# Performance work log

Measured on AMD Instinct MI355X. Metric: run time of the kernel, lower is better.

Reference implementation:

```python
import jax, jax.numpy as jnp
import numpy as np

N_NODES = 500000
EMB = 32
K = 10          # sampled neighbors per node (num_sample in source)
BATCH = 100000


def setup_inputs() -> dict:
    key = jax.random.key(0)
    k1, k2, k3, k4, k5 = jax.random.split(key, 5)
    # xavier-ish scale for weights [emb, 2*emb]
    w_scale = jnp.sqrt(2.0 / (EMB + 2 * EMB)).astype(jnp.float32)
    emb = jax.random.normal(k1, (N_NODES, EMB), dtype=jnp.float32)
    W1 = jax.random.normal(k2, (EMB, 2 * EMB), dtype=jnp.float32) * w_scale
    W2 = jax.random.normal(k3, (EMB, 2 * EMB), dtype=jnp.float32) * w_scale
    node_batch = jax.random.randint(k4, (BATCH,), 0, N_NODES)
    neigh = jax.random.randint(k5, (N_NODES, K), 0, N_NODES)
    return {"emb": emb, "W1": W1, "W2": W2,
            "node_batch": node_batch, "neigh": neigh}


def _sage_layer(self_feat, agg_feat, W):
    # SageLayer.forward: relu(W.mm(cat([self, agg], 1).t()).t()) == relu(cat @ W.T)
    combined = jnp.concatenate([self_feat, agg_feat], axis=1)  # [n, 2E]
    return jax.nn.relu(combined @ W.T)                          # [n, E]


def reference(emb, W1, W2, node_batch, neigh):
    # Layer 1: MEAN aggregation of K sampled neighbors for every node
    # (mask.mm(embed_matrix) with row-normalized 0/1 mask == gather + mean)
    agg1 = jnp.take(emb, neigh, axis=0).mean(axis=1)   # [N, E]
    h1 = _sage_layer(emb, agg1, W1)                    # [N, E]
    # Layer 2: aggregate over neighbors of the batch nodes using layer-1 embeds
    nb_neigh = jnp.take(neigh, node_batch, axis=0)     # [B, K]
    agg2 = jnp.take(h1, nb_neigh, axis=0).mean(axis=1) # [B, E]
    out = _sage_layer(jnp.take(h1, node_batch, axis=0), agg2, W2)  # [B, E]
    return out
```

## Files before the change

kernel.cpp:

```cpp
#include <hip/hip_runtime.h>

#define EMBD 32
#define KN 10

__device__ __forceinline__ float bf2f(unsigned short u) {
    union { unsigned int u; float f; } c; c.u = ((unsigned int)u) << 16; return c.f;
}
__device__ __forceinline__ unsigned short f2bf(float f) {
    union { float f; unsigned int u; } c; c.f = f;
    unsigned int u = c.u + 0x7FFFu + ((c.u >> 16) & 1u);
    return (unsigned short)(u >> 16);
}

__global__ __launch_bounds__(256)
void cvt_bf16_kernel(const float4* __restrict__ in, ushort4* __restrict__ out, int n4)
{
    int i = blockIdx.x * 256 + threadIdx.x;
    if (i < n4) {
        float4 v = in[i];
        ushort4 o;
        o.x = f2bf(v.x); o.y = f2bf(v.y); o.z = f2bf(v.z); o.w = f2bf(v.w);
        out[i] = o;
    }
}

template<bool REMAP, bool OUT_BF16>
__global__ __launch_bounds__(256, 4)
void sage_layer(const unsigned short* __restrict__ feat,
                const float* __restrict__ W,
                const int*   __restrict__ neigh,
                const int*   __restrict__ remap,
                void*        __restrict__ out,
                int n_rows)
{
    __shared__ float sh[64][65];
    const int tid  = threadIdx.x;
    const int row0 = blockIdx.x << 6;

    {
        const int hw = tid >> 5;
        const int j  = tid & 31;
        #pragma unroll 2
        for (int i = 0; i < 8; ++i) {
            const int rl = hw * 8 + i;
            int r = row0 + rl;
            if (r >= n_rows) r = n_rows - 1;
            const int node = REMAP ? remap[r] : r;
            const float self = bf2f(feat[node * EMBD + j]);
            const int* nb = neigh + node * KN;
            float agg = 0.f;
            #pragma unroll
            for (int k = 0; k < KN; ++k)
                agg += bf2f(feat[nb[k] * EMBD + j]);
            sh[j][rl]      = self;
            sh[32 + j][rl] = agg * 0.1f;
        }
    }
    __syncthreads();

    const int row = tid & 63;
    const int wid = __builtin_amdgcn_readfirstlane(tid >> 6);
    const float* Wb = W + wid * 8 * 64;

    float acc[8] = {0.f,0.f,0.f,0.f,0.f,0.f,0.f,0.f};
    #pragma unroll 8
    for (int jj = 0; jj < 64; ++jj) {
        const float c = sh[jj][row];
        #pragma unroll
        for (int q = 0; q < 8; ++q)
            acc[q] = fmaf(c, Wb[q * 64 + jj], acc[q]);
    }

    const int r = row0 + row;
    if (r < n_rows) {
        if (OUT_BF16) {
            unsigned int pk[4];
            #pragma unroll
            for (int q = 0; q < 4; ++q) {
                float a0 = fmaxf(acc[2*q],     0.f);
                float a1 = fmaxf(acc[2*q + 1], 0.f);
                pk[q] = (unsigned int)f2bf(a0) | ((unsigned int)f2bf(a1) << 16);
            }
            uint4* dst = (uint4*)((unsigned short*)out + (size_t)r * EMBD + wid * 8);
            *dst = make_uint4(pk[0], pk[1], pk[2], pk[3]);
        } else {
            float* dst = (float*)out + (size_t)r * EMBD + wid * 8;
            ((float4*)dst)[0] = make_float4(fmaxf(acc[0],0.f), fmaxf(acc[1],0.f),
                                            fmaxf(acc[2],0.f), fmaxf(acc[3],0.f));
            ((float4*)dst)[1] = make_float4(fmaxf(acc[4],0.f), fmaxf(acc[5],0.f),
                                            fmaxf(acc[6],0.f), fmaxf(acc[7],0.f));
        }
    }
}

extern "C" void kernel_launch(void* const* d_in, const int* in_sizes, int n_in,
                              void* d_out, int out_size, void* d_ws, size_t ws_size,
                              hipStream_t stream)
{
    const float* emb        = (const float*)d_in[0];
    const float* W1         = (const float*)d_in[1];
    const float* W2         = (const float*)d_in[2];
    const int*   node_batch = (const int*)  d_in[3];
    const int*   neigh      = (const int*)  d_in[4];

    const int N = in_sizes[0] / EMBD;
    const int B = in_sizes[3];

    unsigned short* emb_bf = (unsigned short*)d_ws;
    unsigned short* h1_bf  = emb_bf + (size_t)N * EMBD;

    const int n4 = (N * EMBD) / 4;
    cvt_bf16_kernel<<<(n4 + 255) / 256, 256, 0, stream>>>(
        (const float4*)emb, (ushort4*)emb_bf, n4);

    sage_layer<false, true><<<(N + 63) / 64, 256, 0, stream>>>(
        emb_bf, W1, neigh, nullptr, (void*)h1_bf, N);

    sage_layer<true, false><<<(B + 63) / 64, 256, 0, stream>>>(
        h1_bf, W2, neigh, node_batch, d_out, B);
}
```

Baseline: 236.5 us.

## Restructure SAGE gathers with staged indices and 8-byte nontemporal row loads

```diff
diff --git a/kernel.cpp b/kernel.cpp
--- a/kernel.cpp
+++ b/kernel.cpp
@@ -3,93 +3,188 @@
 #define EMBD 32
 #define KN 10
 
-__device__ __forceinline__ float bf2f(unsigned short u) {
-    union { unsigned int u; float f; } c; c.u = ((unsigned int)u) << 16; return c.f;
-}
-__device__ __forceinline__ unsigned short f2bf(float f) {
-    union { float f; unsigned int u; } c; c.f = f;
-    unsigned int u = c.u + 0x7FFFu + ((c.u >> 16) & 1u);
-    return (unsigned short)(u >> 16);
+__device__ __forceinline__ float bf_lo(unsigned int u){ union{unsigned int v; float f;}c; c.v = u<<16; return c.f; }
+__device__ __forceinline__ float bf_hi(unsigned int u){ union{unsigned int v; float f;}c; c.v = u & 0xFFFF0000u; return c.f; }
+__device__ __forceinline__ unsigned short f2bf(float f){
+    union{float f; unsigned int u;}c; c.f=f;
+    unsigned int r = c.u + 0x7FFFu + ((c.u>>16)&1u);
+    return (unsigned short)(r>>16);
+}
+__device__ __forceinline__ void ld_nt4bf(const unsigned short* p,
+                                         float& f0, float& f1, float& f2, float& f3){
+    unsigned long long v = __builtin_nontemporal_load((const unsigned long long*)p);
+    unsigned int lo = (unsigned int)v, hi = (unsigned int)(v >> 32);
+    f0 = bf_lo(lo); f1 = bf_hi(lo); f2 = bf_lo(hi); f3 = bf_hi(hi);
 }
 
 __global__ __launch_bounds__(256)
-void cvt_bf16_kernel(const float4* __restrict__ in, ushort4* __restrict__ out, int n4)
+void cvt_bf16(const float4* __restrict__ in, ushort4* __restrict__ out, int n4){
+    int i = blockIdx.x*256 + threadIdx.x;
+    if (i < n4){
+        float4 v = in[i];
+        ushort4 o; o.x=f2bf(v.x); o.y=f2bf(v.y); o.z=f2bf(v.z); o.w=f2bf(v.w);
+        out[i]=o;
+    }
+}
+
+__global__ __launch_bounds__(256, 6)
+void sage_l1(const float* __restrict__ emb,
+             const unsigned short* __restrict__ embb,
+             const float* __restrict__ W,
+             const int* __restrict__ neigh,
+             unsigned short* __restrict__ h1,
+             int n_rows)
 {
-    int i = blockIdx.x * 256 + threadIdx.x;
-    if (i < n4) {
-        float4 v = in[i];
-        ushort4 o;
-        o.x = f2bf(v.x); o.y = f2bf(v.y); o.z = f2bf(v.z); o.w = f2bf(v.w);
-        out[i] = o;
-    }
-}
-
-template<bool REMAP, bool OUT_BF16>
-__global__ __launch_bounds__(256, 4)
-void sage_layer(const unsigned short* __restrict__ feat,
-                const float* __restrict__ W,
-                const int*   __restrict__ neigh,
-                const int*   __restrict__ remap,
-                void*        __restrict__ out,
-                int n_rows)
-{
-    __shared__ float sh[64][65];
+    __shared__ __align__(16) int sidx[64*KN];
+    __shared__ float sagg[64][33];
     const int tid  = threadIdx.x;
     const int row0 = blockIdx.x << 6;
 
-    {
-        const int hw = tid >> 5;
-        const int j  = tid & 31;
-        #pragma unroll 2
-        for (int i = 0; i < 8; ++i) {
-            const int rl = hw * 8 + i;
-            int r = row0 + rl;
-            if (r >= n_rows) r = n_rows - 1;
-            const int node = REMAP ? remap[r] : r;
-            const float self = bf2f(feat[node * EMBD + j]);
-            const int* nb = neigh + node * KN;
-            float agg = 0.f;
-            #pragma unroll
-            for (int k = 0; k < KN; ++k)
-                agg += bf2f(feat[nb[k] * EMBD + j]);
-            sh[j][rl]      = self;
-            sh[32 + j][rl] = agg * 0.1f;
-        }
-    }
-    __syncthreads();
-
-    const int row = tid & 63;
-    const int wid = __builtin_amdgcn_readfirstlane(tid >> 6);
-    const float* Wb = W + wid * 8 * 64;
-
-    float acc[8] = {0.f,0.f,0.f,0.f,0.f,0.f,0.f,0.f};
+    if (row0 + 64 <= n_rows) {
+        if (tid < 160)
+            ((int4*)sidx)[tid] = ((const int4*)(neigh + (size_t)row0*KN))[tid];
+    } else {
+        for (int t = tid; t < 64*KN; t += 256) {
+            int lr = t / KN;
+            sidx[t] = (row0 + lr < n_rows) ? neigh[(size_t)row0*KN + t] : 0;
+        }
+    }
+    __syncthreads();
+
+    const int lane = tid & 63;
+    const int wv   = tid >> 6;
+    const int slot = lane & 7;
+    const int rsub = lane >> 3;
+
+    #pragma unroll
+    for (int gi = 0; gi < 2; ++gi) {
+        const int row = (2*wv + gi)*8 + rsub;
+        float a0=0.f,a1=0.f,a2=0.f,a3=0.f;
+        #pragma unroll
+        for (int k = 0; k < KN; ++k) {
+            const int idx = sidx[row*KN + k];
+            float f0,f1,f2,f3;
+            ld_nt4bf(embb + (size_t)idx*EMBD + slot*4, f0,f1,f2,f3);
+            a0 += f0; a1 += f1; a2 += f2; a3 += f3;
+        }
+        sagg[row][slot*4+0] = a0*0.1f;
+        sagg[row][slot*4+1] = a1*0.1f;
+        sagg[row][slot*4+2] = a2*0.1f;
+        sagg[row][slot*4+3] = a3*0.1f;
+    }
+    __syncthreads();
+
+    const int row = lane;
+    const int r   = row0 + row;
+    const int rc  = (r < n_rows) ? r : (n_rows - 1);
+    const float* selfrow = emb + (size_t)rc * EMBD;
+    const float* Wb = W + wv*8*64;
+
+    float acc[8] = {0,0,0,0,0,0,0,0};
+    #pragma unroll
+    for (int c4 = 0; c4 < 8; ++c4) {
+        const float4 s = ((const float4*)selfrow)[c4];
+        #pragma unroll
+        for (int q = 0; q < 8; ++q) {
+            acc[q] = fmaf(s.x, Wb[q*64 + c4*4 + 0], acc[q]);
+            acc[q] = fmaf(s.y, Wb[q*64 + c4*4 + 1], acc[q]);
+            acc[q] = fmaf(s.z, Wb[q*64 + c4*4 + 2], acc[q]);
+            acc[q] = fmaf(s.w, Wb[q*64 + c4*4 + 3], acc[q]);
+        }
+    }
     #pragma unroll 8
-    for (int jj = 0; jj < 64; ++jj) {
-        const float c = sh[jj][row];
+    for (int j = 0; j < 32; ++j) {
+        const float c = sagg[row][j];
         #pragma unroll
         for (int q = 0; q < 8; ++q)
-            acc[q] = fmaf(c, Wb[q * 64 + jj], acc[q]);
-    }
-
-    const int r = row0 + row;
+            acc[q] = fmaf(c, Wb[q*64 + 32 + j], acc[q]);
+    }
     if (r < n_rows) {
-        if (OUT_BF16) {
-            unsigned int pk[4];
-            #pragma unroll
-            for (int q = 0; q < 4; ++q) {
-                float a0 = fmaxf(acc[2*q],     0.f);
-                float a1 = fmaxf(acc[2*q + 1], 0.f);
-                pk[q] = (unsigned int)f2bf(a0) | ((unsigned int)f2bf(a1) << 16);
-            }
-            uint4* dst = (uint4*)((unsigned short*)out + (size_t)r * EMBD + wid * 8);
-            *dst = make_uint4(pk[0], pk[1], pk[2], pk[3]);
-        } else {
-            float* dst = (float*)out + (size_t)r * EMBD + wid * 8;
-            ((float4*)dst)[0] = make_float4(fmaxf(acc[0],0.f), fmaxf(acc[1],0.f),
-                                            fmaxf(acc[2],0.f), fmaxf(acc[3],0.f));
-            ((float4*)dst)[1] = make_float4(fmaxf(acc[4],0.f), fmaxf(acc[5],0.f),
-                                            fmaxf(acc[6],0.f), fmaxf(acc[7],0.f));
-        }
+        unsigned int pk[4];
+        #pragma unroll
+        for (int q = 0; q < 4; ++q) {
+            float x0 = fmaxf(acc[2*q],0.f), x1 = fmaxf(acc[2*q+1],0.f);
+            pk[q] = (unsigned int)f2bf(x0) | ((unsigned int)f2bf(x1)<<16);
+        }
+        *(uint4*)(h1 + (size_t)r*EMBD + wv*8) = make_uint4(pk[0],pk[1],pk[2],pk[3]);
+    }
+}
+
+__global__ __launch_bounds__(256, 6)
+void sage_l2(const unsigned short* __restrict__ h1,
+             const float* __restrict__ W,
+             const int* __restrict__ neigh,
+             const int* __restrict__ batch,
+             float* __restrict__ out,
+             int n_rows)
+{
+    __shared__ int snode[64];
+    __shared__ __align__(16) int sidx[64*KN];
+    __shared__ float sh[64][67];
+    const int tid  = threadIdx.x;
+    const int row0 = blockIdx.x << 6;
+
+    if (tid < 64) {
+        int r = row0 + tid;
+        snode[tid] = (r < n_rows) ? batch[r] : 0;
+    }
+    __syncthreads();
+    for (int t = tid; t < 64*KN; t += 256) {
+        int lr = t / KN;
+        int k  = t - lr*KN;
+        sidx[t] = neigh[(size_t)snode[lr]*KN + k];
+    }
+    __syncthreads();
+
+    const int lane = tid & 63;
+    const int wv   = tid >> 6;
+    const int slot = lane & 7;
+    const int rsub = lane >> 3;
+
+    #pragma unroll
+    for (int gi = 0; gi < 2; ++gi) {
+        const int row = (2*wv + gi)*8 + rsub;
+        {
+            const int node = snode[row];
+            float f0,f1,f2,f3;
+            ld_nt4bf(h1 + (size_t)node*EMBD + slot*4, f0,f1,f2,f3);
+            sh[row][slot*4+0] = f0;
+            sh[row][slot*4+1] = f1;
+            sh[row][slot*4+2] = f2;
+            sh[row][slot*4+3] = f3;
+        }
+        float a0=0.f,a1=0.f,a2=0.f,a3=0.f;
+        #pragma unroll
+        for (int k = 0; k < KN; ++k) {
+            const int idx = sidx[row*KN + k];
+            float f0,f1,f2,f3;
+            ld_nt4bf(h1 + (size_t)idx*EMBD + slot*4, f0,f1,f2,f3);
+            a0 += f0; a1 += f1; a2 += f2; a3 += f3;
+        }
+        sh[row][32 + slot*4+0] = a0*0.1f;
+        sh[row][32 + slot*4+1] = a1*0.1f;
+        sh[row][32 + slot*4+2] = a2*0.1f;
+        sh[row][32 + slot*4+3] = a3*0.1f;
+    }
+    __syncthreads();
+
+    const int row = lane;
+    const int r   = row0 + row;
+    const float* Wb = W + wv*8*64;
+    float acc[8] = {0,0,0,0,0,0,0,0};
+    #pragma unroll 8
+    for (int j = 0; j < 64; ++j) {
+        const float c = sh[row][j];
+        #pragma unroll
+        for (int q = 0; q < 8; ++q)
+            acc[q] = fmaf(c, Wb[q*64 + j], acc[q]);
+    }
+    if (r < n_rows) {
+        float* dst = out + (size_t)r*EMBD + wv*8;
+        ((float4*)dst)[0] = make_float4(fmaxf(acc[0],0.f),fmaxf(acc[1],0.f),
+                                        fmaxf(acc[2],0.f),fmaxf(acc[3],0.f));
+        ((float4*)dst)[1] = make_float4(fmaxf(acc[4],0.f),fmaxf(acc[5],0.f),
+                                        fmaxf(acc[6],0.f),fmaxf(acc[7],0.f));
     }
 }
 
@@ -110,12 +205,12 @@
     unsigned short* h1_bf  = emb_bf + (size_t)N * EMBD;
 
     const int n4 = (N * EMBD) / 4;
-    cvt_bf16_kernel<<<(n4 + 255) / 256, 256, 0, stream>>>(
+    cvt_bf16<<<(n4 + 255) / 256, 256, 0, stream>>>(
         (const float4*)emb, (ushort4*)emb_bf, n4);
 
-    sage_layer<false, true><<<(N + 63) / 64, 256, 0, stream>>>(
-        emb_bf, W1, neigh, nullptr, (void*)h1_bf, N);
-
-    sage_layer<true, false><<<(B + 63) / 64, 256, 0, stream>>>(
-        h1_bf, W2, neigh, node_batch, d_out, B);
-}
+    sage_l1<<<(N + 63) / 64, 256, 0, stream>>>(
+        emb, emb_bf, W1, neigh, h1_bf, N);
+
+    sage_l2<<<(B + 63) / 64, 256, 0, stream>>>(
+        h1_bf, W2, neigh, node_batch, (float*)d_out, B);
+}
```

Measured after the change: 383.7 us. +62.2%, slower.
